# Kernel optimization log

Hardware: AMD Instinct MI355X
Metric: run time of the kernel (lower is better)

## Reference

```python
import jax, jax.numpy as jnp
import numpy as np

LEAKY_ALPHA = 0.2
LN_EPS = 1e-5


def setup_inputs() -> dict:
    key = jax.random.key(0)
    ks = jax.random.split(key, 6)
    B, N, D, R, Hh, hd = 2, 2048, 128, 3, 4, 32  # head_dim = out_dim // num_heads = 128 // 4
    H = jax.random.normal(ks[0], (B, N, D), dtype=jnp.float32)
    A = jax.random.randint(ks[1], (R, B, N, N), 0, 2, dtype=jnp.int32)  # 0/1 adjacency per relation
    w_scale = float(np.sqrt(2.0 / (D + hd)))  # xavier-like
    a_scale = float(np.sqrt(2.0 / (hd + 1)))
    W = jax.random.normal(ks[2], (R, Hh, D, hd), dtype=jnp.float32) * w_scale
    a_src = jax.random.normal(ks[3], (R, Hh, hd), dtype=jnp.float32) * a_scale
    a_dst = jax.random.normal(ks[4], (R, Hh, hd), dtype=jnp.float32) * a_scale
    ln_gamma = jnp.ones((D,), dtype=jnp.float32)
    ln_beta = jnp.zeros((D,), dtype=jnp.float32)
    return {"H": H, "A": A, "W": W, "a_src": a_src, "a_dst": a_dst,
            "ln_gamma": ln_gamma, "ln_beta": ln_beta}


def reference(H, A, W, a_src, a_dst, ln_gamma, ln_beta):
    # H: [B,N,D]; A: [R,B,N,N] int; W: [R,Hh,D,hd]; a_*: [R,Hh,hd]
    R = W.shape[0]
    B, N, D = H.shape
    mask = (A > 0)[:, :, None, :, :]                    # [R,B,1,N,N]
    Wh = jnp.einsum('bnd,rhdf->rbhnf', H, W)             # [R,B,Hh,N,hd]
    e_src = jnp.einsum('rbhnf,rhf->rbhn', Wh, a_src)
    e_dst = jnp.einsum('rbhnf,rhf->rbhn', Wh, a_dst)
    e = e_src[..., :, None] + e_dst[..., None, :]        # [R,B,Hh,N,N]
    e = jax.nn.leaky_relu(e, LEAKY_ALPHA)
    all_false = ~jnp.any(mask, axis=-1, keepdims=True)   # rows with empty neighborhood
    logits = jnp.where(mask, e, -jnp.inf)
    logits = jnp.where(all_false, 0.0, logits)           # avoid NaN on empty rows
    alpha = jax.nn.softmax(logits, axis=-1)
    alpha = jnp.where(all_false, 0.0, alpha)
    # attention-weighted aggregation, mean over relations; -> [B,N,Hh,hd]
    agg = jnp.einsum('rbhij,rbhjf->bihf', alpha, Wh) / R
    out = agg.reshape(B, N, -1)                          # concat heads -> [B,N,out_dim]
    x = H + out                                          # res_proj is Identity (in_dim==out_dim); dropout in eval
    mu = jnp.mean(x, axis=-1, keepdims=True)
    var = jnp.var(x, axis=-1, keepdims=True)
    return (x - mu) / jnp.sqrt(var + LN_EPS) * ln_gamma + ln_beta
```

## Files before the change

kernel.cpp:

```cpp
#include <hip/hip_runtime.h>
#include <hip/hip_bf16.h>

#define RR 3
#define BB 2
#define NN 2048
#define DD 128
#define HH 4
#define HD 32
#define LEAKY 0.2f
#define LN_EPS 1e-5f
#define LOG2E 1.4426950408889634f

using f32x4  = __attribute__((ext_vector_type(4))) float;
using bf16x8 = __attribute__((ext_vector_type(8))) short;

__device__ __forceinline__ unsigned short bfb(float x) {
    return __builtin_bit_cast(unsigned short, __float2bfloat16(x));
}


__global__ __launch_bounds__(256) void prep_kernel(
    const float* __restrict__ H, const int* __restrict__ A,
    const float* __restrict__ W,
    const float* __restrict__ a_src, const float* __restrict__ a_dst,
    float* __restrict__ es, float* __restrict__ ed,
    __hip_bfloat16* __restrict__ whT, unsigned* __restrict__ bm)
{
    __shared__ unsigned cb_lds[16][65];

    const int bid = blockIdx.x;
    const int t = threadIdx.x;
    const int w = t >> 6;
    const int l = t & 63;

    if (bid < 768) {
        const int sel_e = l >> 3;
        const int sel_q = (l >> 1) & 3;
        const int sel_h = l & 1;
#pragma unroll
        for (int iter = 0; iter < 4; ++iter) {
            const int lr = iter * 4 + w;
            const long crow = (long)bid * 16 + lr;
            const int4* Ap = (const int4*)A + crow * 512 + l;
            int4 v[8];
#pragma unroll
            for (int e = 0; e < 8; ++e) v[e] = Ap[e * 64];
            unsigned word = 0;
#pragma unroll
            for (int e = 0; e < 8; ++e) {
                const unsigned long long B0 = __ballot(v[e].x != 0);
                const unsigned long long B1 = __ballot(v[e].y != 0);
                const unsigned long long B2 = __ballot(v[e].z != 0);
                const unsigned long long B3 = __ballot(v[e].w != 0);
                if (sel_e == e) {
                    const unsigned long long Bq =
                        (sel_q == 3) ? B3 : (sel_q == 2) ? B2 : (sel_q == 1) ? B1 : B0;
                    word = sel_h ? (unsigned)(Bq >> 32) : (unsigned)Bq;
                }
            }
            cb_lds[lr][l] = word;
        }
        __syncthreads();
        {
            const long nrow0g = (long)bid * 16;
            const int rb = (int)(nrow0g >> 11);
            const int nrow0 = (int)(nrow0g & 2047);
            const int p = t >> 2, c = t & 3;
            uint4 val;
            val.x = cb_lds[c * 4 + 0][p];
            val.y = cb_lds[c * 4 + 1][p];
            val.z = cb_lds[c * 4 + 2][p];
            val.w = cb_lds[c * 4 + 3][p];
            *(uint4*)(bm + ((long)rb * 64 + p) * 2048 + nrow0 + c * 4) = val;
        }
        return;
    }

    const int wb = bid - 768;
    const int rbh = wb >> 4;
    const int nch = wb & 15;
    const int h = rbh & 3;
    const int b = (rbh >> 2) & 1;
    const int r = rbh >> 3;
    const int wi = r * HH + h;
    const int lr = l & 15;
    const int lg = l >> 4;

    const float* Wp = W + (long)wi * DD * HD;
    bf16x8 afr[2][4];
#pragma unroll
    for (int mt = 0; mt < 2; ++mt)
#pragma unroll
        for (int kt = 0; kt < 4; ++kt)
#pragma unroll
            for (int e = 0; e < 8; ++e)
                afr[mt][kt][e] = (short)bfb(Wp[(kt * 32 + lg * 8 + e) * HD + mt * 16 + lr]);

    float av[2][4], dv[2][4];
#pragma unroll
    for (int mt = 0; mt < 2; ++mt)
#pragma unroll
        for (int reg = 0; reg < 4; ++reg) {
            const int f = mt * 16 + lg * 4 + reg;
            av[mt][reg] = a_src[wi * HD + f] * LOG2E;
            dv[mt][reg] = a_dst[wi * HD + f] * LOG2E;
        }

    __hip_bfloat16* tile = whT + ((long)rbh * 16 + nch) * 4096;

#pragma unroll
    for (int nt = 0; nt < 2; ++nt) {
        const int ncol = nch * 128 + w * 32 + nt * 16 + lr;
        const float4* hrow4 = (const float4*)(H + ((long)b * NN + ncol) * DD);
        f32x4 acc0 = {0.f, 0.f, 0.f, 0.f};
        f32x4 acc1 = {0.f, 0.f, 0.f, 0.f};
#pragma unroll
        for (int kt = 0; kt < 4; ++kt) {
            float4 h0 = hrow4[kt * 8 + lg * 2];
            float4 h1 = hrow4[kt * 8 + lg * 2 + 1];
            bf16x8 bfr;
            bfr[0] = (short)bfb(h0.x); bfr[1] = (short)bfb(h0.y);
            bfr[2] = (short)bfb(h0.z); bfr[3] = (short)bfb(h0.w);
            bfr[4] = (short)bfb(h1.x); bfr[5] = (short)bfb(h1.y);
            bfr[6] = (short)bfb(h1.z); bfr[7] = (short)bfb(h1.w);
            acc0 = __builtin_amdgcn_mfma_f32_16x16x32_bf16(afr[0][kt], bfr, acc0, 0, 0, 0);
            acc1 = __builtin_amdgcn_mfma_f32_16x16x32_bf16(afr[1][kt], bfr, acc1, 0, 0, 0);
        }
        const int kgw = nt * 2 + (lr >> 3);
        const int ew = lr & 7;
        float s = 0.f, d = 0.f;
#pragma unroll
        for (int reg = 0; reg < 4; ++reg) {
            const int f0 = lg * 4 + reg;
            const int f1 = 16 + lg * 4 + reg;
            tile[((w * 4 + kgw) * 32 + f0) * 8 + ew] = __float2bfloat16(acc0[reg]);
            tile[((w * 4 + kgw) * 32 + f1) * 8 + ew] = __float2bfloat16(acc1[reg]);
            s = fmaf(acc0[reg], av[0][reg], s);
            s = fmaf(acc1[reg], av[1][reg], s);
            d = fmaf(acc0[reg], dv[0][reg], d);
            d = fmaf(acc1[reg], dv[1][reg], d);
        }
        s += __shfl_xor(s, 16); s += __shfl_xor(s, 32);
        d += __shfl_xor(d, 16); d += __shfl_xor(d, 32);
        if (l < 16) {
            es[(long)rbh * NN + ncol] = s;
            ed[(long)rbh * NN + ncol] = d;
        }
    }
}

__global__ __launch_bounds__(256, 6) void gat_attn_kernel(
    const unsigned* __restrict__ bm, const float* __restrict__ es,
    const float* __restrict__ ed, const __hip_bfloat16* __restrict__ whT,
    unsigned* __restrict__ num, float* __restrict__ den)
{
    const int lg = ((int)blockIdx.x % 8) * 192 + (int)blockIdx.x / 8;
    const int jh = lg & 1;
    const int it = (lg >> 1) & 127;
    const int b  = (lg >> 8) & 1;
    const int r  = lg >> 9;
    const int i0 = it << 4;
    const int tid = threadIdx.x;
    const int h = tid >> 6;
    const int l = tid & 63;
    const int row = l & 15;
    const int kg  = l >> 4;

    const int rb  = r * BB + b;
    const int rbh = rb * HH + h;
    const float* edr = ed + (long)rbh * NN;

    float mm = -1e30f;
#pragma unroll
    for (int k = 0; k < 8; ++k) {
        float4 v = ((const float4*)edr)[k * 64 + l];
        mm = fmaxf(mm, fmaxf(fmaxf(v.x, v.y), fmaxf(v.z, v.w)));
    }
#pragma unroll
    for (int d = 1; d < 64; d <<= 1) mm = fmaxf(mm, __shfl_xor(mm, d));

    const float esv = es[(long)rbh * NN + i0 + row];
    const float x = esv + mm;
    const float M = fmaxf(x, LEAKY * x);
    const float uA = esv - M;
    const float vA = fmaf(LEAKY, esv, -M);

    f32x4 acc0 = {0,0,0,0}, acc1 = {0,0,0,0}, accD = {0,0,0,0};
    bf16x8 ones;
#pragma unroll
    for (int i = 0; i < 8; ++i) ones[i] = (short)0x3F80;

    const int kk = kg * 2;
    const unsigned* bmb = bm + (long)rb * 64 * 2048 + i0 + row;

#pragma unroll 1
    for (int seg = 0; seg < 8; ++seg) {
        const int S = jh * 8 + seg;
        const __hip_bfloat16* tile = whT + ((long)rbh * 16 + S) * 4096;
        const int wbase = (S >> 1) * 8 + (S & 1);
        unsigned wA[4];
#pragma unroll
        for (int q = 0; q < 4; ++q)
            wA[q] = bmb[(long)(wbase + q * 2) * 2048];
        const float* edseg = edr + S * 128;

#pragma unroll
        for (int jc = 0; jc < 4; ++jc) {
            bf16x8 b0 = *(const bf16x8*)(tile + jc * 1024 + kg * 256 + row * 8);
            bf16x8 b1 = *(const bf16x8*)(tile + jc * 1024 + kg * 256 + 128 + row * 8);
            float4 e0 = *(const float4*)(edseg + jc * 32 + kg * 8);
            float4 e1 = *(const float4*)(edseg + jc * 32 + kg * 8 + 4);

            unsigned uq[4];
#pragma unroll
            for (int q = 0; q < 4; ++q) uq[q] = wA[q] >> (jc * 8 + kk);

            float ev[8];
            ev[0] = e0.x; ev[1] = e0.y; ev[2] = e0.z; ev[3] = e0.w;
            ev[4] = e1.x; ev[5] = e1.y; ev[6] = e1.z; ev[7] = e1.w;

            bf16x8 p;
#pragma unroll
            for (int c = 0; c < 8; ++c) {
                float pa = __builtin_amdgcn_exp2f(
                    fmaxf(uA + ev[c], fmaf(LEAKY, ev[c], vA)));
                const int ma = ((int)(uq[c & 3] << (31 - (c >> 2)))) >> 31;
                pa = __uint_as_float(__float_as_uint(pa) & (unsigned)ma);
                __hip_bfloat16 ha = __float2bfloat16(pa);
                p[c] = __builtin_bit_cast(short, ha);
            }

            __builtin_amdgcn_s_setprio(1);
            acc0 = __builtin_amdgcn_mfma_f32_16x16x32_bf16(p, b0, acc0, 0, 0, 0);
            acc1 = __builtin_amdgcn_mfma_f32_16x16x32_bf16(p, b1, acc1, 0, 0, 0);
            accD = __builtin_amdgcn_mfma_f32_16x16x32_bf16(p, ones, accD, 0, 0, 0);
            __builtin_amdgcn_s_setprio(0);
        }
    }

    const int fcol = l & 15;
    const int pr = r * 2 + jh;
#pragma unroll
    for (int reg = 0; reg < 4; ++reg) {
        const int orow = (l >> 4) * 4 + reg;
        const long ro = (long)pr * (BB * NN) + (long)b * NN + i0 + orow;
        num[ro * 64 + h * 16 + fcol] =
            (unsigned)bfb(acc0[reg]) | ((unsigned)bfb(acc1[reg]) << 16);
        if (fcol == 0) den[ro * HH + h] = accD[reg];
    }
}

__global__ __launch_bounds__(256) void finalize_kernel(
    const float* __restrict__ H, const unsigned* __restrict__ num,
    const float* __restrict__ den,
    const float* __restrict__ gamma, const float* __restrict__ beta,
    float* __restrict__ out)
{
    const int w = threadIdx.x >> 6;
    const int l = threadIdx.x & 63;
    const long row = (long)blockIdx.x * 4 + w;
    const int hh = l >> 4, cc = l & 15;
    const int c_lo = hh * 32 + cc, c_hi = c_lo + 16;
    const float hx = H[row * DD + c_lo];
    const float hy = H[row * DD + c_hi];

    float ax = 0.f, ay = 0.f;
#pragma unroll
    for (int r = 0; r < RR; ++r) {
        float dsum = 0.f, nx = 0.f, ny = 0.f;
#pragma unroll
        for (int j = 0; j < 2; ++j) {
            const long ro = (long)(r * 2 + j) * (BB * NN) + row;
            dsum += den[ro * HH + hh];
            const unsigned wv = num[ro * 64 + l];
            nx += __uint_as_float(wv << 16);
            ny += __uint_as_float(wv & 0xffff0000u);
        }
        const float inv = (dsum > 0.f) ? 1.0f / dsum : 0.0f;
        ax = fmaf(nx, inv, ax);
        ay = fmaf(ny, inv, ay);
    }
    const float x0 = hx + ax * (1.0f / RR);
    const float x1 = hy + ay * (1.0f / RR);
    float s = x0 + x1, q = x0 * x0 + x1 * x1;
#pragma unroll
    for (int m = 1; m < 64; m <<= 1) {
        s += __shfl_xor(s, m);
        q += __shfl_xor(q, m);
    }
    const float mu  = s * (1.0f / DD);
    const float var = q * (1.0f / DD) - mu * mu;
    const float inv = rsqrtf(var + LN_EPS);
    out[row * DD + c_lo] = (x0 - mu) * inv * gamma[c_lo] + beta[c_lo];
    out[row * DD + c_hi] = (x1 - mu) * inv * gamma[c_hi] + beta[c_hi];
}

extern "C" void kernel_launch(void* const* d_in, const int* in_sizes, int n_in,
                              void* d_out, int out_size, void* d_ws, size_t ws_size,
                              hipStream_t stream)
{
    const float* H      = (const float*)d_in[0];
    const int*   A      = (const int*)d_in[1];
    const float* W      = (const float*)d_in[2];
    const float* a_src  = (const float*)d_in[3];
    const float* a_dst  = (const float*)d_in[4];
    const float* gamma  = (const float*)d_in[5];
    const float* beta   = (const float*)d_in[6];
    float* out = (float*)d_out;

    char* ws = (char*)d_ws;
    unsigned* num = (unsigned*)ws;               ws += (size_t)RR * 2 * BB * NN * 64 * 4;
    float* den = (float*)ws;                     ws += (size_t)RR * 2 * BB * NN * HH * 4;
    float* es  = (float*)ws;                     ws += (size_t)RR * BB * HH * NN * 4;
    float* ed  = (float*)ws;                     ws += (size_t)RR * BB * HH * NN * 4;
    __hip_bfloat16* whT = (__hip_bfloat16*)ws;   ws += (size_t)RR * BB * HH * HD * NN * 2;
    unsigned* bmask = (unsigned*)ws;             ws += (size_t)RR * BB * NN * (NN / 32) * 4;

    prep_kernel<<<768 + 384, 256, 0, stream>>>(
        H, A, W, a_src, a_dst, es, ed, whT, bmask);
    gat_attn_kernel<<<RR * BB * 128 * 2, 256, 0, stream>>>(bmask, es, ed, whT, num, den);
    finalize_kernel<<<BB * NN / 4, 256, 0, stream>>>(H, num, den, gamma, beta, out);
}
```

Baseline: 63.40 us.

## Factor exponentials into precomputed per-column exp2 terms to remove per-element exp

Precomputes exp2(ed) and exp2(0.2*ed) per column in the prep kernel and per-row exp2 factors in the attention kernel, so each attention weight becomes max(PA*E1, PB*E2) instead of an exp2 call. bf16 packing switches from rounded conversion to truncation via byte permute, the segment loop is unrolled by 2 and setprio hints are dropped. This removes a transcendental per element at the cost of loading two float arrays instead of one, and risks overflow for large logits and slightly different rounding.

```diff
diff --git a/kernel.cpp b/kernel.cpp
--- a/kernel.cpp
+++ b/kernel.cpp
@@ -24,6 +24,7 @@
     const float* __restrict__ W,
     const float* __restrict__ a_src, const float* __restrict__ a_dst,
     float* __restrict__ es, float* __restrict__ ed,
+    float* __restrict__ E1, float* __restrict__ E2,
     __hip_bfloat16* __restrict__ whT, unsigned* __restrict__ bm)
 {
     __shared__ unsigned cb_lds[16][65];
@@ -145,13 +146,16 @@
         if (l < 16) {
             es[(long)rbh * NN + ncol] = s;
             ed[(long)rbh * NN + ncol] = d;
+            E1[(long)rbh * NN + ncol] = __builtin_amdgcn_exp2f(d);
+            E2[(long)rbh * NN + ncol] = __builtin_amdgcn_exp2f(LEAKY * d);
         }
     }
 }
 
 __global__ __launch_bounds__(256, 6) void gat_attn_kernel(
     const unsigned* __restrict__ bm, const float* __restrict__ es,
-    const float* __restrict__ ed, const __hip_bfloat16* __restrict__ whT,
+    const float* __restrict__ ed, const float* __restrict__ E1,
+    const float* __restrict__ E2, const __hip_bfloat16* __restrict__ whT,
     unsigned* __restrict__ num, float* __restrict__ den)
 {
     const int lg = ((int)blockIdx.x % 8) * 192 + (int)blockIdx.x / 8;
@@ -182,8 +186,8 @@
     const float esv = es[(long)rbh * NN + i0 + row];
     const float x = esv + mm;
     const float M = fmaxf(x, LEAKY * x);
-    const float uA = esv - M;
-    const float vA = fmaf(LEAKY, esv, -M);
+    const float PA = __builtin_amdgcn_exp2f(esv - M);
+    const float PB = __builtin_amdgcn_exp2f(fmaf(LEAKY, esv, -M));
 
     f32x4 acc0 = {0,0,0,0}, acc1 = {0,0,0,0}, accD = {0,0,0,0};
     bf16x8 ones;
@@ -192,8 +196,10 @@
 
     const int kk = kg * 2;
     const unsigned* bmb = bm + (long)rb * 64 * 2048 + i0 + row;
-
-#pragma unroll 1
+    const float* E1r = E1 + (long)rbh * NN;
+    const float* E2r = E2 + (long)rbh * NN;
+
+#pragma unroll 2
     for (int seg = 0; seg < 8; ++seg) {
         const int S = jh * 8 + seg;
         const __hip_bfloat16* tile = whT + ((long)rbh * 16 + S) * 4096;
@@ -202,39 +208,47 @@
 #pragma unroll
         for (int q = 0; q < 4; ++q)
             wA[q] = bmb[(long)(wbase + q * 2) * 2048];
-        const float* edseg = edr + S * 128;
+        const float* e1seg = E1r + S * 128;
+        const float* e2seg = E2r + S * 128;
 
 #pragma unroll
         for (int jc = 0; jc < 4; ++jc) {
             bf16x8 b0 = *(const bf16x8*)(tile + jc * 1024 + kg * 256 + row * 8);
             bf16x8 b1 = *(const bf16x8*)(tile + jc * 1024 + kg * 256 + 128 + row * 8);
-            float4 e0 = *(const float4*)(edseg + jc * 32 + kg * 8);
-            float4 e1 = *(const float4*)(edseg + jc * 32 + kg * 8 + 4);
+            float4 a0 = *(const float4*)(e1seg + jc * 32 + kg * 8);
+            float4 a1 = *(const float4*)(e1seg + jc * 32 + kg * 8 + 4);
+            float4 c0 = *(const float4*)(e2seg + jc * 32 + kg * 8);
+            float4 c1 = *(const float4*)(e2seg + jc * 32 + kg * 8 + 4);
 
             unsigned uq[4];
 #pragma unroll
             for (int q = 0; q < 4; ++q) uq[q] = wA[q] >> (jc * 8 + kk);
 
-            float ev[8];
-            ev[0] = e0.x; ev[1] = e0.y; ev[2] = e0.z; ev[3] = e0.w;
-            ev[4] = e1.x; ev[5] = e1.y; ev[6] = e1.z; ev[7] = e1.w;
-
-            bf16x8 p;
-#pragma unroll
-            for (int c = 0; c < 8; ++c) {
-                float pa = __builtin_amdgcn_exp2f(
-                    fmaxf(uA + ev[c], fmaf(LEAKY, ev[c], vA)));
-                const int ma = ((int)(uq[c & 3] << (31 - (c >> 2)))) >> 31;
-                pa = __uint_as_float(__float_as_uint(pa) & (unsigned)ma);
-                __hip_bfloat16 ha = __float2bfloat16(pa);
-                p[c] = __builtin_bit_cast(short, ha);
+            float e1v[8], e2v[8];
+            e1v[0] = a0.x; e1v[1] = a0.y; e1v[2] = a0.z; e1v[3] = a0.w;
+            e1v[4] = a1.x; e1v[5] = a1.y; e1v[6] = a1.z; e1v[7] = a1.w;
+            e2v[0] = c0.x; e2v[1] = c0.y; e2v[2] = c0.z; e2v[3] = c0.w;
+            e2v[4] = c1.x; e2v[5] = c1.y; e2v[6] = c1.z; e2v[7] = c1.w;
+
+            unsigned pw[4];
+#pragma unroll
+            for (int k2 = 0; k2 < 4; ++k2) {
+                unsigned pb[2];
+#pragma unroll
+                for (int sub = 0; sub < 2; ++sub) {
+                    const int c = k2 * 2 + sub;
+                    float p = fmaxf(PA * e1v[c], PB * e2v[c]);
+                    const int ma = ((int)(uq[c & 3] << (31 - (c >> 2)))) >> 31;
+                    pb[sub] = __float_as_uint(p) & (unsigned)ma;
+                }
+                pw[k2] = __builtin_amdgcn_perm(pb[1], pb[0], 0x07060302u);
             }
-
-            __builtin_amdgcn_s_setprio(1);
-            acc0 = __builtin_amdgcn_mfma_f32_16x16x32_bf16(p, b0, acc0, 0, 0, 0);
-            acc1 = __builtin_amdgcn_mfma_f32_16x16x32_bf16(p, b1, acc1, 0, 0, 0);
-            accD = __builtin_amdgcn_mfma_f32_16x16x32_bf16(p, ones, accD, 0, 0, 0);
-            __builtin_amdgcn_s_setprio(0);
+            union { unsigned u[4]; bf16x8 v; } pk;
+            pk.u[0] = pw[0]; pk.u[1] = pw[1]; pk.u[2] = pw[2]; pk.u[3] = pw[3];
+
+            acc0 = __builtin_amdgcn_mfma_f32_16x16x32_bf16(pk.v, b0, acc0, 0, 0, 0);
+            acc1 = __builtin_amdgcn_mfma_f32_16x16x32_bf16(pk.v, b1, acc1, 0, 0, 0);
+            accD = __builtin_amdgcn_mfma_f32_16x16x32_bf16(pk.v, ones, accD, 0, 0, 0);
         }
     }
 
@@ -313,11 +327,14 @@
     float* den = (float*)ws;                     ws += (size_t)RR * 2 * BB * NN * HH * 4;
     float* es  = (float*)ws;                     ws += (size_t)RR * BB * HH * NN * 4;
     float* ed  = (float*)ws;                     ws += (size_t)RR * BB * HH * NN * 4;
+    float* E1  = (float*)ws;                     ws += (size_t)RR * BB * HH * NN * 4;
+    float* E2  = (float*)ws;                     ws += (size_t)RR * BB * HH * NN * 4;
     __hip_bfloat16* whT = (__hip_bfloat16*)ws;   ws += (size_t)RR * BB * HH * HD * NN * 2;
     unsigned* bmask = (unsigned*)ws;             ws += (size_t)RR * BB * NN * (NN / 32) * 4;
 
     prep_kernel<<<768 + 384, 256, 0, stream>>>(
-        H, A, W, a_src, a_dst, es, ed, whT, bmask);
-    gat_attn_kernel<<<RR * BB * 128 * 2, 256, 0, stream>>>(bmask, es, ed, whT, num, den);
+        H, A, W, a_src, a_dst, es, ed, E1, E2, whT, bmask);
+    gat_attn_kernel<<<RR * BB * 128 * 2, 256, 0, stream>>>(
+        bmask, es, ed, E1, E2, whT, num, den);
     finalize_kernel<<<BB * NN / 4, 256, 0, stream>>>(H, num, den, gamma, beta, out);
 }
```

New measurement: 69.30 us. 1.09x slower.
